# Kernel tuning notes

Hardware: AMD Instinct MI355X
Metric: run time of the kernel (lower is better)

The kernel has to match this reference:

```python
import jax, jax.numpy as jnp
import numpy as np

D_MODEL = 256; N_HEADS = 8; N_LAYERS = 6; D_FF = 1024; BATCH = 1
INPUT_SHAPES = [(24, 24, 24), (12, 12, 12), (6, 6, 6)]
NUM_ORGANS = 20; QPO = 5; LEVELS = 3
NUM_PATCHES = [int(np.prod(s)) for s in INPUT_SHAPES]
S_TOTAL = int(sum(NUM_PATCHES))          # 15768 flattened multi-level patches
NUM_Q = QPO * LEVELS * NUM_ORGANS        # 300 queries


def _build_attn_mask():
    # Same structure as FocusedAttnDecoder.generate_attn_mask: per-organ
    # normalized bbox, scaled (floor/ceil) into each feature level, queries
    # ordered organ-major then level then query copy. True = blocked.
    rng = np.random.RandomState(0)
    mask = np.ones((NUM_Q, S_TOTAL), dtype=bool)
    offsets = np.cumsum([0] + NUM_PATCHES[:-1])
    qi = 0
    for organ in range(NUM_ORGANS):
        lo = rng.uniform(0.0, 0.5, 3)
        hi = np.minimum(lo + rng.uniform(0.15, 0.45, 3), 1.0)
        for lvl in range(LEVELS):
            shp = np.array(INPUT_SHAPES[lvl])
            a = np.floor(lo * shp).astype(int)
            b = np.ceil(hi * shp).astype(int)
            dummy = np.zeros(INPUT_SHAPES[lvl], dtype=bool)
            dummy[a[0]:b[0], a[1]:b[1], a[2]:b[2]] = True
            idx = np.nonzero(dummy.ravel())[0] + offsets[lvl]
            for _ in range(QPO):
                mask[qi, idx] = False
                qi += 1
    return mask


def _xavier(key, shape):
    fan_in, fan_out = shape[-1], shape[-2]
    lim = float(np.sqrt(6.0 / (fan_in + fan_out)))
    return jax.random.uniform(key, shape, minval=-lim, maxval=lim, dtype=jnp.float32)


def setup_inputs() -> dict:
    key = jax.random.key(0)
    ks = jax.random.split(key, 9)
    L, C, F = N_LAYERS, D_MODEL, D_FF
    return {
        "srcs": jax.random.normal(ks[0], (BATCH, C, S_TOTAL), jnp.float32),
        "pos_embeds": jax.random.normal(ks[1], (BATCH, C, S_TOTAL), jnp.float32),
        "query_embed": jax.random.normal(ks[2], (NUM_Q, 2 * C), jnp.float32),
        "attn_mask": jnp.asarray(_build_attn_mask()),
        "sa_in_w": _xavier(ks[3], (L, 3 * C, C)), "sa_in_b": jnp.zeros((L, 3 * C), jnp.float32),
        "sa_out_w": _xavier(ks[4], (L, C, C)), "sa_out_b": jnp.zeros((L, C), jnp.float32),
        "ca_in_w": _xavier(ks[5], (L, 3 * C, C)), "ca_in_b": jnp.zeros((L, 3 * C), jnp.float32),
        "ca_out_w": _xavier(ks[6], (L, C, C)), "ca_out_b": jnp.zeros((L, C), jnp.float32),
        "ln1_w": jnp.ones((L, C), jnp.float32), "ln1_b": jnp.zeros((L, C), jnp.float32),
        "ln2_w": jnp.ones((L, C), jnp.float32), "ln2_b": jnp.zeros((L, C), jnp.float32),
        "ln3_w": jnp.ones((L, C), jnp.float32), "ln3_b": jnp.zeros((L, C), jnp.float32),
        "ff1_w": _xavier(ks[7], (L, F, C)), "ff1_b": jnp.zeros((L, F), jnp.float32),
        "ff2_w": _xavier(ks[8], (L, C, F)), "ff2_b": jnp.zeros((L, C), jnp.float32),
    }


def _ln(x, w, b, eps=1e-5):
    m = jnp.mean(x, axis=-1, keepdims=True)
    v = jnp.mean(jnp.square(x - m), axis=-1, keepdims=True)
    return (x - m) * jax.lax.rsqrt(v + eps) * w + b


def _mha(q_in, k_in, v_in, in_w, in_b, out_w, out_b, mask=None):
    # Faithful nn.MultiheadAttention (eval mode): packed in_proj, scale q,
    # additive -inf mask (True = blocked), softmax, out_proj.
    B, Lq, C = q_in.shape
    H = N_HEADS; Dh = C // H
    wq, wk, wv = jnp.split(in_w, 3, axis=0)
    bq, bk, bv = jnp.split(in_b, 3)
    q = (q_in @ wq.T + bq) * (Dh ** -0.5)
    k = k_in @ wk.T + bk
    v = v_in @ wv.T + bv
    q = q.reshape(B, Lq, H, Dh)
    k = k.reshape(B, k_in.shape[1], H, Dh)
    v = v.reshape(B, v_in.shape[1], H, Dh)
    scores = jnp.einsum('bqhd,bkhd->bhqk', q, k)
    if mask is not None:
        scores = jnp.where(mask[None, None], -jnp.inf, scores)
    attn = jax.nn.softmax(scores, axis=-1)
    out = jnp.einsum('bhqk,bkhd->bqhd', attn, v).reshape(B, Lq, C)
    return out @ out_w.T + out_b


def reference(srcs, pos_embeds, query_embed, attn_mask,
              sa_in_w, sa_in_b, sa_out_w, sa_out_b,
              ca_in_w, ca_in_b, ca_out_w, ca_out_b,
              ln1_w, ln1_b, ln2_w, ln2_b, ln3_w, ln3_b,
              ff1_w, ff1_b, ff2_w, ff2_b):
    C = D_MODEL
    src = jnp.transpose(srcs, (0, 2, 1))        # [B, S, C]
    pos = jnp.transpose(pos_embeds, (0, 2, 1))  # [B, S, C]
    B = src.shape[0]
    qe = jnp.broadcast_to(query_embed[:, :C], (B, NUM_Q, C))
    x = jnp.broadcast_to(query_embed[:, C:], (B, NUM_Q, C))
    for l in range(N_LAYERS):
        # self-attention over queries (q/k get query_pos, v is raw tgt)
        qk = x + qe
        sa = _mha(qk, qk, x, sa_in_w[l], sa_in_b[l], sa_out_w[l], sa_out_b[l])
        x = _ln(x + sa, ln2_w[l], ln2_b[l])
        # mask-restricted cross-attention over flattened multi-level src
        ca = _mha(x + qe, src + pos, src,
                  ca_in_w[l], ca_in_b[l], ca_out_w[l], ca_out_b[l], mask=attn_mask)
        x = _ln(x + ca, ln1_w[l], ln1_b[l])
        # FFN
        h = jax.nn.relu(x @ ff1_w[l].T + ff1_b[l])
        x = _ln(x + (h @ ff2_w[l].T + ff2_b[l]), ln3_w[l], ln3_b[l])
    return x
```

## Files before the change

kernel.cpp:

```cpp
#include <hip/hip_runtime.h>
#include <hip/hip_bf16.h>
#include <math.h>

#define S_TOTAL 15768
#define NQ 300
#define C 256
#define H 8
#define DH 32
#define FF 1024
#define NL 6
#define MAXN 1792
#define NROW 60
#define NT_MAX 16384
#define MQ16 19

#define WB_SAW   0u
#define WB_SAOW  1179648u
#define WB_CAW   1572864u
#define WB_CAOW  2752512u
#define WB_FF1   3145728u
#define WB_FF2   4718592u
#define WB_SAB   6291456u
#define WB_SAOB  6296064u
#define WB_CAB   6297600u
#define WB_CAOB  6302208u
#define WB_FF1B  6303744u
#define WB_FF2B  6309888u
#define WB_TOT   6311424u
#define WT_SAOW  6311424u
#define WT_CAOW  6704640u
#define WB_TOT2  7097856u
#define WT_ELEMS 786432u

typedef __hip_bfloat16 bf16;
typedef __attribute__((ext_vector_type(8))) short bf16x8;
typedef __attribute__((ext_vector_type(4))) float f32x4;

__device__ __forceinline__ float b2f(bf16 v){ return __bfloat162float(v); }

__device__ __forceinline__ float ldin(const void* p, size_t i, int isbf){
    if (isbf) return b2f(((const bf16*)p)[i]);
    return ((const float*)p)[i];
}

__device__ __forceinline__ short f2bf_s(float v){
    bf16 h = __float2bfloat16(v);
    return *(short*)&h;
}

__device__ __forceinline__ float s2f(unsigned short s){
    union { unsigned u; float f; } w; w.u = ((unsigned)s) << 16; return w.f;
}

__device__ __forceinline__ bf16x8 f8_to_bf(float4 a, float4 b){
    bf16x8 r;
    r[0]=f2bf_s(a.x); r[1]=f2bf_s(a.y); r[2]=f2bf_s(a.z); r[3]=f2bf_s(a.w);
    r[4]=f2bf_s(b.x); r[5]=f2bf_s(b.y); r[6]=f2bf_s(b.z); r[7]=f2bf_s(b.w);
    return r;
}


__global__ void detect_cfg(const uint4* __restrict__ srcs,
                           const uint4* __restrict__ mask,
                           int* __restrict__ cfg){
    __shared__ int red[256];
    int t = threadIdx.x;
    int c = 0;
    for (int i = t; i < 16384; i += 256){
        uint4 v = srcs[i];
        unsigned w0 = v.x, w1 = v.y, w2 = v.z, w3 = v.w;
        if ((w0 & 0x7F80u) == 0x7F80u) c++;
        if (((w0 >> 16) & 0x7F80u) == 0x7F80u) c++;
        if ((w1 & 0x7F80u) == 0x7F80u) c++;
        if (((w1 >> 16) & 0x7F80u) == 0x7F80u) c++;
        if ((w2 & 0x7F80u) == 0x7F80u) c++;
        if (((w2 >> 16) & 0x7F80u) == 0x7F80u) c++;
        if ((w3 & 0x7F80u) == 0x7F80u) c++;
        if (((w3 >> 16) & 0x7F80u) == 0x7F80u) c++;
    }
    red[t] = c; __syncthreads();
    for (int s = 128; s > 0; s >>= 1){ if (t < s) red[t] += red[t+s]; __syncthreads(); }
    if (t == 0) cfg[0] = (red[0] >= 16) ? 0 : 1;
    __syncthreads();
    int c2 = 0;
    for (int i = t; i < 4096; i += 256){
        uint4 v = mask[i];
        unsigned w[4] = {v.x, v.y, v.z, v.w};
        #pragma unroll
        for (int j = 0; j < 4; j++){
            unsigned x = w[j];
            c2 += ((x & 0xFFu) != 0) + (((x >> 8) & 0xFFu) != 0)
                + (((x >> 16) & 0xFFu) != 0) + (((x >> 24) & 0xFFu) != 0);
        }
    }
    red[t] = c2; __syncthreads();
    for (int s = 128; s > 0; s >>= 1){ if (t < s) red[t] += red[t+s]; __syncthreads(); }
    if (t == 0) cfg[1] = (red[0] > 32768) ? 1 : 0;
}


__global__ void convert_all(
    const void* saw, const void* sab, const void* saow, const void* saob,
    const void* caw, const void* cab, const void* caow, const void* caob,
    const void* f1w, const void* f1b, const void* f2w, const void* f2b,
    const int* __restrict__ cfg, bf16* __restrict__ Wb)
{
    int isbf = cfg[0];
    size_t i = ((size_t)blockIdx.x*256 + threadIdx.x) * 4;
    if (i >= WB_TOT) return;
    const void* src; size_t loc;
    if      (i < WB_SAOW){ src = saw;  loc = i - WB_SAW; }
    else if (i < WB_CAW) { src = saow; loc = i - WB_SAOW; }
    else if (i < WB_CAOW){ src = caw;  loc = i - WB_CAW; }
    else if (i < WB_FF1) { src = caow; loc = i - WB_CAOW; }
    else if (i < WB_FF2) { src = f1w;  loc = i - WB_FF1; }
    else if (i < WB_SAB) { src = f2w;  loc = i - WB_FF2; }
    else if (i < WB_SAOB){ src = sab;  loc = i - WB_SAB; }
    else if (i < WB_CAB) { src = saob; loc = i - WB_SAOB; }
    else if (i < WB_CAOB){ src = cab;  loc = i - WB_CAB; }
    else if (i < WB_FF1B){ src = caob; loc = i - WB_CAOB; }
    else if (i < WB_FF2B){ src = f1b;  loc = i - WB_FF1B; }
    else                 { src = f2b;  loc = i - WB_FF2B; }
    #pragma unroll
    for (int t = 0; t < 4; t++)
        Wb[i+t] = __float2bfloat16(ldin(src, loc+t, isbf));
}


__global__ void build_wt(bf16* __restrict__ Wb){
    unsigned i = blockIdx.x*256 + threadIdx.x;
    if (i >= WT_ELEMS) return;
    if (i < 393216u){
        unsigned l = i / 65536u, r = i % 65536u, k = r >> 8, n = r & 255u;
        Wb[WT_SAOW + i] = Wb[WB_SAOW + l*65536u + n*256u + k];
    } else {
        unsigned j = i - 393216u;
        unsigned l = j / 65536u, r = j % 65536u, k = r >> 8, n = r & 255u;
        Wb[WT_CAOW + j] = Wb[WB_CAOW + l*65536u + n*256u + k];
    }
}


__global__ void init_qx(const void* __restrict__ qemb, const int* __restrict__ cfg,
                        float* __restrict__ qe, float* __restrict__ x){
    int isbf = cfg[0];
    int i = blockIdx.x*256 + threadIdx.x;
    if (i >= NQ*C) return;
    int row = i / C, col = i % C;
    qe[i] = ldin(qemb, (size_t)row*2*C + col, isbf);
    x[i]  = ldin(qemb, (size_t)row*2*C + C + col, isbf);
}

__global__ void write_out(const float* __restrict__ x, const int* __restrict__ cfg,
                          void* __restrict__ o){
    int isbf = cfg[0];
    int i = blockIdx.x*256 + threadIdx.x;
    if (i >= NQ*C) return;
    if (isbf) ((bf16*)o)[i] = __float2bfloat16(x[i]);
    else      ((float*)o)[i] = x[i];
}


__global__ void count_rows(const unsigned char* __restrict__ mask8,
                           const int* __restrict__ cfg, int* __restrict__ rcnt){
    __shared__ int red[256];
    int r = blockIdx.x;
    int t = threadIdx.x;
    bool isbyte = (cfg[1] != 0);
    const int* row32 = (const int*)mask8 + (size_t)(r*5) * S_TOTAL;
    const unsigned char* row8 = mask8 + (size_t)(r*5) * S_TOTAL;
    int c = 0;
    for (int s = t; s < S_TOTAL; s += 256){
        int blocked = isbyte ? (int)row8[s] : row32[s];
        if (blocked == 0) c++;
    }
    red[t] = c; __syncthreads();
    for (int s = 128; s > 0; s >>= 1){ if (t < s) red[t] += red[t+s]; __syncthreads(); }
    if (t == 0) rcnt[r] = min(red[0], MAXN);
}

__global__ void prefix_rows(const int* __restrict__ rcnt, int* __restrict__ off){
    if (threadIdx.x == 0){
        int a = 0;
        for (int r = 0; r < NROW; r++){
            off[r] = a;
            a = min(a + rcnt[r], NT_MAX);
        }
        off[NROW] = a;
    }
}

__global__ void fill_glist(const unsigned char* __restrict__ mask8,
                           const int* __restrict__ cfg, const int* __restrict__ off,
                           int* __restrict__ glist){
    __shared__ int counts[257];
    int r = blockIdx.x;
    int t = threadIdx.x;
    bool isbyte = (cfg[1] != 0);
    const int* row32 = (const int*)mask8 + (size_t)(r*5) * S_TOTAL;
    const unsigned char* row8 = mask8 + (size_t)(r*5) * S_TOTAL;
    const int chunk = (S_TOTAL + 255) / 256;
    int s0 = t*chunk, s1 = min(S_TOTAL, s0+chunk);
    int c = 0;
    for (int s = s0; s < s1; s++){
        int blocked = isbyte ? (int)row8[s] : row32[s];
        if (blocked == 0) c++;
    }
    counts[t+1] = c;
    __syncthreads();
    if (t == 0){
        counts[0] = 0;
        for (int i = 1; i <= 256; i++) counts[i] += counts[i-1];
    }
    __syncthreads();
    int o = off[r] + counts[t];
    int lim = off[r+1];
    for (int s = s0; s < s1; s++){
        int blocked = isbyte ? (int)row8[s] : row32[s];
        if (blocked == 0){ if (o < lim) glist[o] = s; o++; }
    }
}


__global__ __launch_bounds__(256) void gather_cast(
    const void* __restrict__ srcs, const void* __restrict__ pos,
    const int* __restrict__ cfg, const int* __restrict__ glist,
    const int* __restrict__ off,
    bf16* __restrict__ Agkv, bf16* __restrict__ Agsrc)
{
    int NT = off[NROW];
    int m0 = blockIdx.x * 64;
    if (m0 >= NT) return;
    int isbf = cfg[0];
    __shared__ __align__(16) short Tkv[64][40];
    __shared__ __align__(16) short Tsr[64][40];
    int tid = threadIdx.x;
    int am = tid & 63;
    int kg = (tid >> 6) * 8;
    int mg = m0 + am;
    int g = (mg < NT) ? glist[mg] : 0;
    int wn = tid >> 2;
    int wk = (tid & 3) * 8;
    bool wvalid = (m0 + wn < NT);
    for (int k0 = 0; k0 < C; k0 += 32){
        #pragma unroll
        for (int i = 0; i < 8; i++){
            int k = k0 + kg + i;
            float s  = ldin(srcs, (size_t)k*S_TOTAL + g, isbf);
            float pp = ldin(pos,  (size_t)k*S_TOTAL + g, isbf);
            Tsr[am][kg+i] = f2bf_s(s);
            Tkv[am][kg+i] = f2bf_s(s + pp);
        }
        __syncthreads();
        if (wvalid){
            *(bf16x8*)(Agkv  + (size_t)(m0+wn)*C + k0 + wk) = *(const bf16x8*)&Tkv[wn][wk];
            *(bf16x8*)(Agsrc + (size_t)(m0+wn)*C + k0 + wk) = *(const bf16x8*)&Tsr[wn][wk];
        }
        __syncthreads();
    }
}


__global__ __launch_bounds__(256) void gemm_kv3(
    const bf16* __restrict__ Agkv, const bf16* __restrict__ Agsrc,
    const bf16* __restrict__ Wb, int lstart,
    const int* __restrict__ off, bf16* __restrict__ KV)
{
    int NT = off[NROW];
    int m0 = blockIdx.x * 128;
    if (m0 >= NT) return;
    int z = blockIdx.z;
    int l = lstart + (z >> 1);
    int kv = z & 1;
    const bf16* Ag = kv ? Agsrc : Agkv;
    size_t woff = WB_CAW + ((size_t)l*3 + 1 + kv) * C * C;
    size_t boff = WB_CAB + ((size_t)l*3 + 1 + kv) * C;
    bf16* Out = KV + (size_t)z * NT_MAX * C;
    int n0 = blockIdx.y * 128;
    int tid = threadIdx.x;
    int lane = tid & 63, wid = tid >> 6;
    int fr = lane & 15, quad = lane >> 4;
    int mbase = (wid & 1) * 64, nbase = (wid >> 1) * 64;

    __shared__ __align__(16) short As[128][72];
    __shared__ __align__(16) short Bs[128][72];

    f32x4 acc[4][4];
    #pragma unroll
    for (int i = 0; i < 4; i++)
        #pragma unroll
        for (int j = 0; j < 4; j++) acc[i][j] = (f32x4)(0.f);

    for (int k0 = 0; k0 < C; k0 += 64){
        #pragma unroll
        for (int it = 0; it < 4; it++){
            int idx = tid + it*256;
            int row = idx >> 3;
            int kseg = (idx & 7) * 8;
            *(bf16x8*)&As[row][kseg] = *(const bf16x8*)(Ag + (size_t)(m0+row)*C + k0 + kseg);
            *(bf16x8*)&Bs[row][kseg] = *(const bf16x8*)(Wb + woff + (size_t)(n0+row)*C + k0 + kseg);
        }
        __syncthreads();
        #pragma unroll
        for (int h = 0; h < 2; h++){
            bf16x8 af[4], bfr[4];
            #pragma unroll
            for (int i = 0; i < 4; i++) af[i] = *(const bf16x8*)&As[mbase+i*16+fr][h*32 + quad*8];
            #pragma unroll
            for (int j = 0; j < 4; j++) bfr[j] = *(const bf16x8*)&Bs[nbase+j*16+fr][h*32 + quad*8];
            #pragma unroll
            for (int i = 0; i < 4; i++)
                #pragma unroll
                for (int j = 0; j < 4; j++)
                    acc[i][j] = __builtin_amdgcn_mfma_f32_16x16x32_bf16(af[i], bfr[j], acc[i][j], 0, 0, 0);
        }
        __syncthreads();
    }

    int col16 = lane & 15, rq = quad * 4;
    #pragma unroll
    for (int j = 0; j < 4; j++){
        int gn = n0 + nbase + j*16 + col16;
        float bv = b2f(Wb[boff + gn]);
        #pragma unroll
        for (int i = 0; i < 4; i++){
            #pragma unroll
            for (int r = 0; r < 4; r++){
                int gm2 = m0 + mbase + i*16 + rq + r;
                if (gm2 < NT) Out[(size_t)gm2*C + gn] = __float2bfloat16(acc[i][j][r] + bv);
            }
        }
    }
}


__global__ __launch_bounds__(64) void gemm_q_mfma(
    const float* __restrict__ A, const float* __restrict__ A2, int a2_nlimit,
    int lda, const bf16* __restrict__ W, size_t woff,
    size_t boff, float* __restrict__ Out,
    int M, int N, int K, int relu)
{
    int lane = threadIdx.x;
    int m0 = blockIdx.x * 16, n0 = blockIdx.y * 16;
    int fr = lane & 15, quad = lane >> 4;
    int gm = m0 + fr;
    int n  = n0 + fr;
    bool mrow = (gm < M);
    bool use2 = (A2 != nullptr) && (n0 < a2_nlimit);
    f32x4 acc = (f32x4)(0.f);

    for (int k0 = 0; k0 < K; k0 += 32){
        bf16x8 af = (bf16x8)(short)0;
        if (mrow){
            const float4* pa = (const float4*)(A + (size_t)gm*lda + k0 + quad*8);
            float4 a0 = pa[0], a1 = pa[1];
            if (use2){
                const float4* p2 = (const float4*)(A2 + (size_t)gm*lda + k0 + quad*8);
                float4 b0 = p2[0], b1 = p2[1];
                a0.x += b0.x; a0.y += b0.y; a0.z += b0.z; a0.w += b0.w;
                a1.x += b1.x; a1.y += b1.y; a1.z += b1.z; a1.w += b1.w;
            }
            af = f8_to_bf(a0, a1);
        }
        bf16x8 bf_ = *(const bf16x8*)(W + woff + (size_t)n*K + k0 + quad*8);
        acc = __builtin_amdgcn_mfma_f32_16x16x32_bf16(af, bf_, acc, 0, 0, 0);
    }

    int col = n0 + (lane & 15);
    int rq = quad * 4;
    float bv = b2f(W[boff + col]);
    #pragma unroll
    for (int r = 0; r < 4; r++){
        int gmr = m0 + rq + r;
        if (gmr < M){
            float v = acc[r] + bv;
            if (relu) v = fmaxf(v, 0.f);
            Out[(size_t)gmr*N + col] = v;
        }
    }
}


__global__ __launch_bounds__(256) void row_out_ln(
    const float* __restrict__ A, const bf16* __restrict__ Wb,
    size_t wtoff, size_t boff,
    const void* __restrict__ lnw, const void* __restrict__ lnb, size_t lnoff,
    const int* __restrict__ cfg, float* __restrict__ x)
{
    int isbf = cfg[0];
    int row = blockIdx.x;
    int tid = threadIdx.x;
    int lane = tid & 63, wv = tid >> 6;
    __shared__ float as[C];
    __shared__ float wsum[4], wsq[4];
    as[tid] = A[(size_t)row*C + tid];
    __syncthreads();
    const bf16* wt = Wb + wtoff;
    float a0=0.f, a1=0.f, a2=0.f, a3=0.f;
    #pragma unroll 4
    for (int k = 0; k < C; k += 4){
        a0 += as[k]   * b2f(wt[(size_t)k*256 + tid]);
        a1 += as[k+1] * b2f(wt[(size_t)(k+1)*256 + tid]);
        a2 += as[k+2] * b2f(wt[(size_t)(k+2)*256 + tid]);
        a3 += as[k+3] * b2f(wt[(size_t)(k+3)*256 + tid]);
    }
    float v = (a0+a1) + (a2+a3) + b2f(Wb[boff + tid]) + x[(size_t)row*C + tid];
    float s = v, q = v*v;
    #pragma unroll
    for (int m = 1; m < 64; m <<= 1){
        s += __shfl_xor(s, m);
        q += __shfl_xor(q, m);
    }
    if (lane == 0){ wsum[wv] = s; wsq[wv] = q; }
    __syncthreads();
    float S = wsum[0]+wsum[1]+wsum[2]+wsum[3];
    float Q = wsq[0]+wsq[1]+wsq[2]+wsq[3];
    float mean = S * (1.f/256.f);
    float var  = Q * (1.f/256.f) - mean*mean;
    float r = (v - mean) * rsqrtf(var + 1e-5f);
    x[(size_t)row*C + tid] = r * ldin(lnw, lnoff+tid, isbf) + ldin(lnb, lnoff+tid, isbf);
}


__global__ void sa_attn(const float* __restrict__ qkv, float* __restrict__ out){
    int qi = blockIdx.x, h = blockIdx.y;
    int lane = threadIdx.x;
    __shared__ __align__(16) float qv[DH];
    __shared__ float sc[NQ];
    const float scale = 0.17677669529663687f;
    if (lane < DH) qv[lane] = qkv[qi*768 + h*DH + lane] * scale;
    __syncthreads();
    float mx = -1e30f;
    const float4* q4 = (const float4*)qv;
    for (int j = lane; j < NQ; j += 64){
        const float4* kp = (const float4*)(qkv + j*768 + 256 + h*DH);
        float d = 0.f;
        #pragma unroll
        for (int b = 0; b < 8; b++){
            float4 kk = kp[b];
            float4 qq = q4[b];
            d += qq.x*kk.x + qq.y*kk.y + qq.z*kk.z + qq.w*kk.w;
        }
        sc[j] = d; mx = fmaxf(mx, d);
    }
    for (int m = 1; m < 64; m <<= 1) mx = fmaxf(mx, __shfl_xor(mx, m));
    float sum = 0.f;
    __syncthreads();
    for (int j = lane; j < NQ; j += 64){ float e = __expf(sc[j]-mx); sc[j] = e; sum += e; }
    for (int m = 1; m < 64; m <<= 1) sum += __shfl_xor(sum, m);
    __syncthreads();
    int dd8 = lane & 3, grp = lane >> 2;
    float acc[8];
    #pragma unroll
    for (int t = 0; t < 8; t++) acc[t] = 0.f;
    for (int j = grp; j < NQ; j += 16){
        const float4* vp = (const float4*)(qkv + j*768 + 512 + h*DH + dd8*8);
        float4 v0 = vp[0], v1 = vp[1];
        float s = sc[j];
        acc[0] += s*v0.x; acc[1] += s*v0.y; acc[2] += s*v0.z; acc[3] += s*v0.w;
        acc[4] += s*v1.x; acc[5] += s*v1.y; acc[6] += s*v1.z; acc[7] += s*v1.w;
    }
    #pragma unroll
    for (int t = 0; t < 8; t++){
        float a = acc[t];
        a += __shfl_xor(a, 4); a += __shfl_xor(a, 8);
        a += __shfl_xor(a, 16); a += __shfl_xor(a, 32);
        acc[t] = a;
    }
    if (lane < 4){
        float inv = 1.f/sum;
        #pragma unroll
        for (int t = 0; t < 8; t++)
            out[qi*C + h*DH + dd8*8 + t] = acc[t]*inv;
    }
}


__global__ __launch_bounds__(256) void ca_attn(
    const float* __restrict__ q, const bf16* __restrict__ Kg,
    const bf16* __restrict__ Vg, const int* __restrict__ off,
    float* __restrict__ out)
{
    int r = blockIdx.x, h = blockIdx.y;
    int tid = threadIdx.x;
    int lane = tid & 63, wv = tid >> 6;
    int base = off[r], n = off[r+1] - base;
    __shared__ __align__(16) float qv[5][DH];
    __shared__ float sc[5][MAXN];
    __shared__ float wred[5][4];
    __shared__ float wsum[5][4];
    __shared__ float pacc[4][5][DH];
    const float scale = 0.17677669529663687f;
    for (int i = tid; i < 5*DH; i += 256){
        int qc = i >> 5, d = i & 31;
        qv[qc][d] = q[(size_t)(r*5+qc)*C + h*DH + d] * scale;
    }
    __syncthreads();
    float mx[5] = {-1e30f,-1e30f,-1e30f,-1e30f,-1e30f};
    for (int ki = tid; ki < n; ki += 256){
        const bf16x8* kp = (const bf16x8*)(Kg + (size_t)(base+ki)*C + h*DH);
        float kf[32];
        #pragma unroll
        for (int b = 0; b < 4; b++){
            bf16x8 k8 = kp[b];
            #pragma unroll
            for (int t = 0; t < 8; t++) kf[b*8+t] = s2f((unsigned short)k8[t]);
        }
        #pragma unroll
        for (int qc = 0; qc < 5; qc++){
            const float4* q4 = (const float4*)qv[qc];
            float d = 0.f;
            #pragma unroll
            for (int b = 0; b < 8; b++){
                float4 qq = q4[b];
                d += qq.x*kf[b*4] + qq.y*kf[b*4+1] + qq.z*kf[b*4+2] + qq.w*kf[b*4+3];
            }
            sc[qc][ki] = d;
            mx[qc] = fmaxf(mx[qc], d);
        }
    }
    #pragma unroll
    for (int qc = 0; qc < 5; qc++)
        for (int m = 1; m < 64; m <<= 1) mx[qc] = fmaxf(mx[qc], __shfl_xor(mx[qc], m));
    if (lane == 0){
        #pragma unroll
        for (int qc = 0; qc < 5; qc++) wred[qc][wv] = mx[qc];
    }
    __syncthreads();
    #pragma unroll
    for (int qc = 0; qc < 5; qc++)
        mx[qc] = fmaxf(fmaxf(wred[qc][0], wred[qc][1]), fmaxf(wred[qc][2], wred[qc][3]));
    float sum[5] = {0.f,0.f,0.f,0.f,0.f};
    for (int ki = tid; ki < n; ki += 256){
        #pragma unroll
        for (int qc = 0; qc < 5; qc++){
            float e = __expf(sc[qc][ki] - mx[qc]);
            sc[qc][ki] = e;
            sum[qc] += e;
        }
    }
    #pragma unroll
    for (int qc = 0; qc < 5; qc++)
        for (int m = 1; m < 64; m <<= 1) sum[qc] += __shfl_xor(sum[qc], m);
    if (lane == 0){
        #pragma unroll
        for (int qc = 0; qc < 5; qc++) wsum[qc][wv] = sum[qc];
    }
    __syncthreads();
    #pragma unroll
    for (int qc = 0; qc < 5; qc++)
        sum[qc] = wsum[qc][0] + wsum[qc][1] + wsum[qc][2] + wsum[qc][3];
    int dd8 = tid & 3, grp = tid >> 2;
    float acc[5][8];
    #pragma unroll
    for (int qc = 0; qc < 5; qc++)
        #pragma unroll
        for (int t = 0; t < 8; t++) acc[qc][t] = 0.f;
    for (int j = grp; j < n; j += 64){
        bf16x8 v8 = *(const bf16x8*)(Vg + (size_t)(base+j)*C + h*DH + dd8*8);
        float vf[8];
        #pragma unroll
        for (int t = 0; t < 8; t++) vf[t] = s2f((unsigned short)v8[t]);
        #pragma unroll
        for (int qc = 0; qc < 5; qc++){
            float s = sc[qc][j];
            #pragma unroll
            for (int t = 0; t < 8; t++) acc[qc][t] += s*vf[t];
        }
    }
    #pragma unroll
    for (int qc = 0; qc < 5; qc++)
        #pragma unroll
        for (int t = 0; t < 8; t++){
            float a = acc[qc][t];
            a += __shfl_xor(a, 4); a += __shfl_xor(a, 8);
            a += __shfl_xor(a, 16); a += __shfl_xor(a, 32);
            acc[qc][t] = a;
        }
    if (lane < 4){
        #pragma unroll
        for (int qc = 0; qc < 5; qc++)
            #pragma unroll
            for (int t = 0; t < 8; t++) pacc[wv][qc][dd8*8+t] = acc[qc][t];
    }
    __syncthreads();
    if (tid < 5*DH){
        int qc = tid >> 5, d = tid & 31;
        float a = pacc[0][qc][d] + pacc[1][qc][d] + pacc[2][qc][d] + pacc[3][qc][d];
        float inv = (n > 0 && sum[qc] > 0.f) ? 1.f/sum[qc] : 0.f;
        out[(size_t)(r*5+qc)*C + h*DH + d] = a*inv;
    }
}


__global__ void add_res_ln(float* __restrict__ x, const float* __restrict__ t,
                           const void* __restrict__ w, const void* __restrict__ b,
                           size_t off, const int* __restrict__ cfg){
    int isbf = cfg[0];
    int row = blockIdx.x;
    int tid = threadIdx.x;
    int lane = tid & 63, wv = tid >> 6;
    __shared__ float wsum[4], wsq[4];
    float v = x[row*C + tid] + t[row*C + tid];
    float s = v, q = v*v;
    #pragma unroll
    for (int m = 1; m < 64; m <<= 1){
        s += __shfl_xor(s, m);
        q += __shfl_xor(q, m);
    }
    if (lane == 0){ wsum[wv] = s; wsq[wv] = q; }
    __syncthreads();
    float S = wsum[0]+wsum[1]+wsum[2]+wsum[3];
    float Q = wsq[0]+wsq[1]+wsq[2]+wsq[3];
    float mean = S * (1.f/256.f);
    float var  = Q * (1.f/256.f) - mean*mean;
    float r = (v - mean) * rsqrtf(var + 1e-5f);
    x[row*C + tid] = r * ldin(w, off + tid, isbf) + ldin(b, off + tid, isbf);
}


extern "C" void kernel_launch(void* const* d_in, const int* in_sizes, int n_in,
                              void* d_out, int out_size, void* d_ws, size_t ws_size,
                              hipStream_t stream) {
    const void* srcs    = d_in[0];
    const void* pos     = d_in[1];
    const void* qemb    = d_in[2];
    const unsigned char* mask = (const unsigned char*)d_in[3];
    const void* sa_in_w = d_in[4];
    const void* sa_in_b = d_in[5];
    const void* sa_out_w= d_in[6];
    const void* sa_out_b= d_in[7];
    const void* ca_in_w = d_in[8];
    const void* ca_in_b = d_in[9];
    const void* ca_out_w= d_in[10];
    const void* ca_out_b= d_in[11];
    const void* ln1_w   = d_in[12];
    const void* ln1_b   = d_in[13];
    const void* ln2_w   = d_in[14];
    const void* ln2_b   = d_in[15];
    const void* ln3_w   = d_in[16];
    const void* ln3_b   = d_in[17];
    const void* ff1_w   = d_in[18];
    const void* ff1_b   = d_in[19];
    const void* ff2_w   = d_in[20];
    const void* ff2_b   = d_in[21];

    const size_t SLICE = (size_t)NT_MAX * C / 2;

    float* p = (float*)d_ws;
    float* qe    = p; p += NQ*C;
    float* x     = p; p += NQ*C;
    bf16*  Agkv  = (bf16*)p; p += SLICE;
    bf16*  Agsrc = (bf16*)p; p += SLICE;
    bf16*  Wb    = (bf16*)p; p += (WB_TOT2+2)/2;
    float* saqkv = p; p += NQ*768;
    float* att   = p; p += NQ*C;
    float* tmp   = p; p += NQ*C;
    float* hbuf  = p; p += NQ*FF;
    float* qbuf  = p; p += NQ*C;
    int*   glist = (int*)p; p += NT_MAX;
    int*   rcnt  = (int*)p; p += NROW;
    int*   off   = (int*)p; p += NROW+4;
    int*   cfg   = (int*)p; p += 4;
    bf16*  KV    = (bf16*)p;

    size_t base_bytes = (size_t)((char*)KV - (char*)d_ws);
    bool hoist = (ws_size >= base_bytes + 12 * SLICE * sizeof(float));

    dim3 blk(256);
    const size_t CC = (size_t)C*C;

    detect_cfg<<<1, blk, 0, stream>>>((const uint4*)srcs, (const uint4*)mask, cfg);
    convert_all<<<(WB_TOT/4 + 255)/256, blk, 0, stream>>>(
        sa_in_w, sa_in_b, sa_out_w, sa_out_b, ca_in_w, ca_in_b, ca_out_w, ca_out_b,
        ff1_w, ff1_b, ff2_w, ff2_b, cfg, Wb);
    build_wt<<<(WT_ELEMS + 255)/256, blk, 0, stream>>>(Wb);
    init_qx<<<(NQ*C+255)/256, blk, 0, stream>>>(qemb, cfg, qe, x);
    count_rows<<<NROW, blk, 0, stream>>>(mask, cfg, rcnt);
    prefix_rows<<<1, 64, 0, stream>>>(rcnt, off);
    fill_glist<<<NROW, blk, 0, stream>>>(mask, cfg, off, glist);
    gather_cast<<<NT_MAX/64, blk, 0, stream>>>(srcs, pos, cfg, glist, off, Agkv, Agsrc);

    if (hoist){
        gemm_kv3<<<dim3(NT_MAX/128, 2, 2*NL), blk, 0, stream>>>(
            Agkv, Agsrc, Wb, 0, off, KV);
    }

    for (int l = 0; l < NL; l++){
        bf16* Kg; bf16* Vg;
        if (hoist){
            Kg = KV + (size_t)(2*l)   * NT_MAX * C;
            Vg = KV + (size_t)(2*l+1) * NT_MAX * C;
        } else {
            Kg = KV;
            Vg = KV + (size_t)NT_MAX * C;
            gemm_kv3<<<dim3(NT_MAX/128, 2, 2), blk, 0, stream>>>(
                Agkv, Agsrc, Wb, l, off, KV);
        }

        gemm_q_mfma<<<dim3(MQ16, 48), 64, 0, stream>>>(
            x, qe, 512, C, Wb, WB_SAW + (size_t)l*3*CC, WB_SAB + (size_t)l*3*C,
            saqkv, NQ, 768, C, 0);
        sa_attn<<<dim3(NQ, H), 64, 0, stream>>>(saqkv, att);
        row_out_ln<<<NQ, blk, 0, stream>>>(
            att, Wb, WT_SAOW + (size_t)l*CC, WB_SAOB + (size_t)l*C,
            ln2_w, ln2_b, (size_t)l*C, cfg, x);

        gemm_q_mfma<<<dim3(MQ16, 16), 64, 0, stream>>>(
            x, qe, 256, C, Wb, WB_CAW + (size_t)l*3*CC, WB_CAB + (size_t)l*3*C,
            qbuf, NQ, 256, C, 0);
        ca_attn<<<dim3(NROW, H), blk, 0, stream>>>(qbuf, Kg, Vg, off, att);
        row_out_ln<<<NQ, blk, 0, stream>>>(
            att, Wb, WT_CAOW + (size_t)l*CC, WB_CAOB + (size_t)l*C,
            ln1_w, ln1_b, (size_t)l*C, cfg, x);

        gemm_q_mfma<<<dim3(MQ16, 64), 64, 0, stream>>>(
            x, nullptr, 0, C, Wb, WB_FF1 + (size_t)l*FF*C, WB_FF1B + (size_t)l*FF,
            hbuf, NQ, FF, C, 1);
        gemm_q_mfma<<<dim3(MQ16, 16), 64, 0, stream>>>(
            hbuf, nullptr, 0, FF, Wb, WB_FF2 + (size_t)l*C*FF, WB_FF2B + (size_t)l*C,
            tmp, NQ, C, FF, 0);
        add_res_ln<<<NQ, blk, 0, stream>>>(x, tmp, ln3_w, ln3_b, (size_t)l*C, cfg);
    }

    write_out<<<(NQ*C+255)/256, blk, 0, stream>>>(x, cfg, d_out);
}
```

Before: 915.7 us.

## Fuse all decoder layers into one persistent kernel with a software grid barrier

Replaces the per-layer sequence of many small kernel launches with a single persistent kernel of 512 blocks. The blocks step through the self-attention, cross-attention, FFN and layernorm phases and synchronize through a hierarchical atomic grid barrier. Self-attention and its output projection plus layernorm are merged into one per-query pass. This targets launch overhead and idle gaps between the tiny per-layer kernels. The cost is barrier spin time, less parallelism in some phases, and a risk of deadlock if all 512 blocks cannot be resident at once.

```diff
diff --git a/kernel.cpp b/kernel.cpp
--- a/kernel.cpp
+++ b/kernel.cpp
@@ -13,6 +13,7 @@
 #define NROW 60
 #define NT_MAX 16384
 #define MQ16 19
+#define GRID 512
 
 #define WB_SAW   0u
 #define WB_SAOW  1179648u
@@ -179,7 +180,9 @@
     if (t == 0) rcnt[r] = min(red[0], MAXN);
 }
 
-__global__ void prefix_rows(const int* __restrict__ rcnt, int* __restrict__ off){
+__global__ void prefix_rows(const int* __restrict__ rcnt, int* __restrict__ off,
+                            int* __restrict__ bar){
+    for (int i = threadIdx.x; i < 160; i += 64) bar[i] = 0;
     if (threadIdx.x == 0){
         int a = 0;
         for (int r = 0; r < NROW; r++){
@@ -334,14 +337,12 @@
 }
 
 
-__global__ __launch_bounds__(64) void gemm_q_mfma(
+__device__ __forceinline__ void gemm_tile16(
     const float* __restrict__ A, const float* __restrict__ A2, int a2_nlimit,
-    int lda, const bf16* __restrict__ W, size_t woff,
-    size_t boff, float* __restrict__ Out,
-    int M, int N, int K, int relu)
+    int lda, const bf16* __restrict__ W, size_t woff, size_t boff,
+    float* __restrict__ Out, int M, int N, int K, int relu,
+    int m0, int n0, int lane)
 {
-    int lane = threadIdx.x;
-    int m0 = blockIdx.x * 16, n0 = blockIdx.y * 16;
     int fr = lane & 15, quad = lane >> 4;
     int gm = m0 + fr;
     int n  = n0 + fr;
@@ -366,20 +367,63 @@
         acc = __builtin_amdgcn_mfma_f32_16x16x32_bf16(af, bf_, acc, 0, 0, 0);
     }
 
-    int col = n0 + (lane & 15);
+    float bv = b2f(W[boff + n]);
     int rq = quad * 4;
-    float bv = b2f(W[boff + col]);
     #pragma unroll
     for (int r = 0; r < 4; r++){
         int gmr = m0 + rq + r;
         if (gmr < M){
             float v = acc[r] + bv;
             if (relu) v = fmaxf(v, 0.f);
-            Out[(size_t)gmr*N + col] = v;
-        }
-    }
-}
-
+            Out[(size_t)gmr*N + n] = v;
+        }
+    }
+}
+
+
+__global__ __launch_bounds__(64) void gemm_q_mfma(
+    const float* __restrict__ A, const float* __restrict__ A2, int a2_nlimit,
+    int lda, const bf16* __restrict__ W, size_t woff,
+    size_t boff, float* __restrict__ Out,
+    int M, int N, int K, int relu)
+{
+    gemm_tile16(A, A2, a2_nlimit, lda, W, woff, boff, Out, M, N, K, relu,
+                blockIdx.x * 16, blockIdx.y * 16, (int)threadIdx.x);
+}
+
+
+__device__ __forceinline__ void out_ln_row(
+    const float* __restrict__ arow, const bf16* __restrict__ Wb,
+    size_t wtoff, size_t boff,
+    const void* __restrict__ lnw, const void* __restrict__ lnb, size_t lnoff,
+    int isbf, float* __restrict__ x, int row, int tid, float* __restrict__ red)
+{
+    int lane = tid & 63, wvv = tid >> 6;
+    const bf16* wt = Wb + wtoff;
+    float a0=0.f, a1=0.f, a2=0.f, a3=0.f;
+    #pragma unroll 4
+    for (int k = 0; k < C; k += 4){
+        a0 += arow[k]   * b2f(wt[(size_t)k*256 + tid]);
+        a1 += arow[k+1] * b2f(wt[(size_t)(k+1)*256 + tid]);
+        a2 += arow[k+2] * b2f(wt[(size_t)(k+2)*256 + tid]);
+        a3 += arow[k+3] * b2f(wt[(size_t)(k+3)*256 + tid]);
+    }
+    float v = (a0+a1) + (a2+a3) + b2f(Wb[boff + tid]) + x[(size_t)row*C + tid];
+    float s = v, q = v*v;
+    #pragma unroll
+    for (int m = 1; m < 64; m <<= 1){
+        s += __shfl_xor(s, m);
+        q += __shfl_xor(q, m);
+    }
+    if (lane == 0){ red[wvv] = s; red[4+wvv] = q; }
+    __syncthreads();
+    float S = red[0]+red[1]+red[2]+red[3];
+    float Q = red[4]+red[5]+red[6]+red[7];
+    float mean = S * (1.f/256.f);
+    float var  = Q * (1.f/256.f) - mean*mean;
+    float r = (v - mean) * rsqrtf(var + 1e-5f);
+    x[(size_t)row*C + tid] = r * ldin(lnw, lnoff+tid, isbf) + ldin(lnb, lnoff+tid, isbf);
+}
 
 __global__ __launch_bounds__(256) void row_out_ln(
     const float* __restrict__ A, const bf16* __restrict__ Wb,
@@ -387,38 +431,13 @@
     const void* __restrict__ lnw, const void* __restrict__ lnb, size_t lnoff,
     const int* __restrict__ cfg, float* __restrict__ x)
 {
-    int isbf = cfg[0];
     int row = blockIdx.x;
     int tid = threadIdx.x;
-    int lane = tid & 63, wv = tid >> 6;
     __shared__ float as[C];
-    __shared__ float wsum[4], wsq[4];
+    __shared__ float red[8];
     as[tid] = A[(size_t)row*C + tid];
     __syncthreads();
-    const bf16* wt = Wb + wtoff;
-    float a0=0.f, a1=0.f, a2=0.f, a3=0.f;
-    #pragma unroll 4
-    for (int k = 0; k < C; k += 4){
-        a0 += as[k]   * b2f(wt[(size_t)k*256 + tid]);
-        a1 += as[k+1] * b2f(wt[(size_t)(k+1)*256 + tid]);
-        a2 += as[k+2] * b2f(wt[(size_t)(k+2)*256 + tid]);
-        a3 += as[k+3] * b2f(wt[(size_t)(k+3)*256 + tid]);
-    }
-    float v = (a0+a1) + (a2+a3) + b2f(Wb[boff + tid]) + x[(size_t)row*C + tid];
-    float s = v, q = v*v;
-    #pragma unroll
-    for (int m = 1; m < 64; m <<= 1){
-        s += __shfl_xor(s, m);
-        q += __shfl_xor(q, m);
-    }
-    if (lane == 0){ wsum[wv] = s; wsq[wv] = q; }
-    __syncthreads();
-    float S = wsum[0]+wsum[1]+wsum[2]+wsum[3];
-    float Q = wsq[0]+wsq[1]+wsq[2]+wsq[3];
-    float mean = S * (1.f/256.f);
-    float var  = Q * (1.f/256.f) - mean*mean;
-    float r = (v - mean) * rsqrtf(var + 1e-5f);
-    x[(size_t)row*C + tid] = r * ldin(lnw, lnoff+tid, isbf) + ldin(lnb, lnoff+tid, isbf);
+    out_ln_row(as, Wb, wtoff, boff, lnw, lnb, lnoff, cfg[0], x, row, tid, red);
 }
 
 
@@ -616,6 +635,310 @@
     float var  = Q * (1.f/256.f) - mean*mean;
     float r = (v - mean) * rsqrtf(var + 1e-5f);
     x[row*C + tid] = r * ldin(w, off + tid, isbf) + ldin(b, off + tid, isbf);
+}
+
+
+__device__ __forceinline__ void gsync(int* __restrict__ bar){
+    __syncthreads();
+    if (threadIdx.x == 0){
+        int g = __hip_atomic_load(bar + 144, __ATOMIC_RELAXED, __HIP_MEMORY_SCOPE_AGENT);
+        int sc_ = (blockIdx.x & 7) << 4;
+        int a = __hip_atomic_fetch_add(bar + sc_, 1, __ATOMIC_ACQ_REL, __HIP_MEMORY_SCOPE_AGENT);
+        if (a == (GRID/8) - 1){
+            __hip_atomic_store(bar + sc_, 0, __ATOMIC_RELAXED, __HIP_MEMORY_SCOPE_AGENT);
+            int m = __hip_atomic_fetch_add(bar + 128, 1, __ATOMIC_ACQ_REL, __HIP_MEMORY_SCOPE_AGENT);
+            if (m == 7){
+                __hip_atomic_store(bar + 128, 0, __ATOMIC_RELAXED, __HIP_MEMORY_SCOPE_AGENT);
+                __hip_atomic_fetch_add(bar + 144, 1, __ATOMIC_ACQ_REL, __HIP_MEMORY_SCOPE_AGENT);
+            }
+        }
+        while (__hip_atomic_load(bar + 144, __ATOMIC_RELAXED, __HIP_MEMORY_SCOPE_AGENT) == g)
+            __builtin_amdgcn_s_sleep(4);
+        (void)__hip_atomic_load(bar + 144, __ATOMIC_ACQUIRE, __HIP_MEMORY_SCOPE_AGENT);
+    }
+    __syncthreads();
+}
+
+union __align__(16) ShU {
+    struct { float qv[8][DH]; float as[C]; float red[8]; } sa;
+    struct { float as[C]; float red[8]; } ro;
+    struct { float qv[5][DH]; float sc[5][MAXN]; float wred[5][4];
+             float wsum[5][4]; float pacc[4][5][DH]; } ca;
+};
+
+__global__ __launch_bounds__(256, 2) void fused_layers(
+    const void* __restrict__ qemb, const int* __restrict__ cfg,
+    const bf16* __restrict__ Wb, const int* __restrict__ off,
+    const bf16* __restrict__ KV,
+    const void* __restrict__ ln1w, const void* __restrict__ ln1b,
+    const void* __restrict__ ln2w, const void* __restrict__ ln2b,
+    const void* __restrict__ ln3w, const void* __restrict__ ln3b,
+    float* __restrict__ qe, float* __restrict__ x,
+    float* __restrict__ saqkv, float* __restrict__ att,
+    float* __restrict__ qbuf, float* __restrict__ hbuf, float* __restrict__ tmp,
+    int* __restrict__ bar, void* __restrict__ outp)
+{
+    __shared__ ShU sh;
+    int tid = threadIdx.x, bid = blockIdx.x;
+    int lane = tid & 63, wv = tid >> 6;
+    int gw = (bid << 2) | wv;
+    int isbf = cfg[0];
+    const float scale = 0.17677669529663687f;
+    const size_t CC = (size_t)C*C;
+
+    for (int i = bid*256 + tid; i < NQ*C; i += GRID*256){
+        int row = i >> 8, col = i & 255;
+        qe[i] = ldin(qemb, (size_t)row*2*C + col, isbf);
+        x[i]  = ldin(qemb, (size_t)row*2*C + C + col, isbf);
+    }
+    gsync(bar);
+
+    for (int l = 0; l < NL; l++){
+        for (int t = gw; t < 19*48; t += GRID*4)
+            gemm_tile16(x, qe, 512, C, Wb, WB_SAW + (size_t)l*3*CC, WB_SAB + (size_t)l*3*C,
+                        saqkv, NQ, 768, C, 0, (t % 19)*16, (t / 19)*16, lane);
+        gsync(bar);
+
+        for (int q = bid; q < NQ; q += GRID){
+            {
+                int h2 = tid >> 5, d = tid & 31;
+                sh.sa.qv[h2][d] = saqkv[(size_t)q*768 + h2*DH + d] * scale;
+            }
+            __syncthreads();
+            #pragma unroll
+            for (int hh = 0; hh < 2; hh++){
+                int h = wv*2 + hh;
+                float e[5]; float mx = -1e30f;
+                #pragma unroll
+                for (int i = 0; i < 5; i++){
+                    int j = lane + 64*i;
+                    float d = -1e30f;
+                    if (j < NQ){
+                        const float4* kp = (const float4*)(saqkv + (size_t)j*768 + 256 + h*DH);
+                        const float4* q4 = (const float4*)sh.sa.qv[h];
+                        d = 0.f;
+                        #pragma unroll
+                        for (int b = 0; b < 8; b++){
+                            float4 kk = kp[b], qq = q4[b];
+                            d += qq.x*kk.x + qq.y*kk.y + qq.z*kk.z + qq.w*kk.w;
+                        }
+                    }
+                    e[i] = d; mx = fmaxf(mx, d);
+                }
+                #pragma unroll
+                for (int m = 1; m < 64; m <<= 1) mx = fmaxf(mx, __shfl_xor(mx, m));
+                float sum = 0.f;
+                #pragma unroll
+                for (int i = 0; i < 5; i++){
+                    int j = lane + 64*i;
+                    float ee = (j < NQ) ? __expf(e[i] - mx) : 0.f;
+                    e[i] = ee; sum += ee;
+                }
+                #pragma unroll
+                for (int m = 1; m < 64; m <<= 1) sum += __shfl_xor(sum, m);
+                int dd8 = lane & 3, grp = lane >> 2;
+                float acc[8];
+                #pragma unroll
+                for (int t = 0; t < 8; t++) acc[t] = 0.f;
+                #pragma unroll
+                for (int k = 0; k < 19; k++){
+                    int j = grp + 16*k;
+                    float s = __shfl(e[k>>2], j & 63);
+                    if (j < NQ){
+                        const float4* vp = (const float4*)(saqkv + (size_t)j*768 + 512 + h*DH + dd8*8);
+                        float4 v0 = vp[0], v1 = vp[1];
+                        acc[0] += s*v0.x; acc[1] += s*v0.y; acc[2] += s*v0.z; acc[3] += s*v0.w;
+                        acc[4] += s*v1.x; acc[5] += s*v1.y; acc[6] += s*v1.z; acc[7] += s*v1.w;
+                    }
+                }
+                #pragma unroll
+                for (int t = 0; t < 8; t++){
+                    float a = acc[t];
+                    a += __shfl_xor(a, 4); a += __shfl_xor(a, 8);
+                    a += __shfl_xor(a, 16); a += __shfl_xor(a, 32);
+                    acc[t] = a;
+                }
+                if (lane < 4){
+                    float inv = 1.f/sum;
+                    #pragma unroll
+                    for (int t = 0; t < 8; t++)
+                        sh.sa.as[h*DH + dd8*8 + t] = acc[t]*inv;
+                }
+            }
+            __syncthreads();
+            out_ln_row(sh.sa.as, Wb, WT_SAOW + (size_t)l*CC, WB_SAOB + (size_t)l*C,
+                       ln2w, ln2b, (size_t)l*C, isbf, x, q, tid, sh.sa.red);
+            __syncthreads();
+        }
+        gsync(bar);
+
+        for (int t = gw; t < 19*16; t += GRID*4)
+            gemm_tile16(x, qe, 256, C, Wb, WB_CAW + (size_t)l*3*CC, WB_CAB + (size_t)l*3*C,
+                        qbuf, NQ, 256, C, 0, (t % 19)*16, (t / 19)*16, lane);
+        gsync(bar);
+
+        {
+            const bf16* Kg = KV + (size_t)(2*l)   * NT_MAX * C;
+            const bf16* Vg = KV + (size_t)(2*l+1) * NT_MAX * C;
+            for (int u = bid; u < NROW*H; u += GRID){
+                int r = u >> 3, h = u & 7;
+                int base = off[r], n = off[r+1] - base;
+                for (int i = tid; i < 5*DH; i += 256){
+                    int qc = i >> 5, d = i & 31;
+                    sh.ca.qv[qc][d] = qbuf[(size_t)(r*5+qc)*C + h*DH + d] * scale;
+                }
+                __syncthreads();
+                float mx[5] = {-1e30f,-1e30f,-1e30f,-1e30f,-1e30f};
+                for (int ki = tid; ki < n; ki += 256){
+                    const bf16x8* kp = (const bf16x8*)(Kg + (size_t)(base+ki)*C + h*DH);
+                    float kf[32];
+                    #pragma unroll
+                    for (int b = 0; b < 4; b++){
+                        bf16x8 k8 = kp[b];
+                        #pragma unroll
+                        for (int t = 0; t < 8; t++) kf[b*8+t] = s2f((unsigned short)k8[t]);
+                    }
+                    #pragma unroll
+                    for (int qc = 0; qc < 5; qc++){
+                        const float4* q4 = (const float4*)sh.ca.qv[qc];
+                        float d = 0.f;
+                        #pragma unroll
+                        for (int b = 0; b < 8; b++){
+                            float4 qq = q4[b];
+                            d += qq.x*kf[b*4] + qq.y*kf[b*4+1] + qq.z*kf[b*4+2] + qq.w*kf[b*4+3];
+                        }
+                        sh.ca.sc[qc][ki] = d;
+                        mx[qc] = fmaxf(mx[qc], d);
+                    }
+                }
+                #pragma unroll
+                for (int qc = 0; qc < 5; qc++)
+                    for (int m = 1; m < 64; m <<= 1) mx[qc] = fmaxf(mx[qc], __shfl_xor(mx[qc], m));
+                if (lane == 0){
+                    #pragma unroll
+                    for (int qc = 0; qc < 5; qc++) sh.ca.wred[qc][wv] = mx[qc];
+                }
+                __syncthreads();
+                #pragma unroll
+                for (int qc = 0; qc < 5; qc++)
+                    mx[qc] = fmaxf(fmaxf(sh.ca.wred[qc][0], sh.ca.wred[qc][1]),
+                                   fmaxf(sh.ca.wred[qc][2], sh.ca.wred[qc][3]));
+                float sum[5] = {0.f,0.f,0.f,0.f,0.f};
+                for (int ki = tid; ki < n; ki += 256){
+                    #pragma unroll
+                    for (int qc = 0; qc < 5; qc++){
+                        float e = __expf(sh.ca.sc[qc][ki] - mx[qc]);
+                        sh.ca.sc[qc][ki] = e;
+                        sum[qc] += e;
+                    }
+                }
+                #pragma unroll
+                for (int qc = 0; qc < 5; qc++)
+                    for (int m = 1; m < 64; m <<= 1) sum[qc] += __shfl_xor(sum[qc], m);
+                if (lane == 0){
+                    #pragma unroll
+                    for (int qc = 0; qc < 5; qc++) sh.ca.wsum[qc][wv] = sum[qc];
+                }
+                __syncthreads();
+                #pragma unroll
+                for (int qc = 0; qc < 5; qc++)
+                    sum[qc] = sh.ca.wsum[qc][0] + sh.ca.wsum[qc][1]
+                            + sh.ca.wsum[qc][2] + sh.ca.wsum[qc][3];
+                int dd8 = tid & 3, grp = tid >> 2;
+                float acc[5][8];
+                #pragma unroll
+                for (int qc = 0; qc < 5; qc++)
+                    #pragma unroll
+                    for (int t = 0; t < 8; t++) acc[qc][t] = 0.f;
+                for (int j = grp; j < n; j += 64){
+                    bf16x8 v8 = *(const bf16x8*)(Vg + (size_t)(base+j)*C + h*DH + dd8*8);
+                    float vf[8];
+                    #pragma unroll
+                    for (int t = 0; t < 8; t++) vf[t] = s2f((unsigned short)v8[t]);
+                    #pragma unroll
+                    for (int qc = 0; qc < 5; qc++){
+                        float s = sh.ca.sc[qc][j];
+                        #pragma unroll
+                        for (int t = 0; t < 8; t++) acc[qc][t] += s*vf[t];
+                    }
+                }
+                #pragma unroll
+                for (int qc = 0; qc < 5; qc++)
+                    #pragma unroll
+                    for (int t = 0; t < 8; t++){
+                        float a = acc[qc][t];
+                        a += __shfl_xor(a, 4); a += __shfl_xor(a, 8);
+                        a += __shfl_xor(a, 16); a += __shfl_xor(a, 32);
+                        acc[qc][t] = a;
+                    }
+                if (lane < 4){
+                    #pragma unroll
+                    for (int qc = 0; qc < 5; qc++)
+                        #pragma unroll
+                        for (int t = 0; t < 8; t++) sh.ca.pacc[wv][qc][dd8*8+t] = acc[qc][t];
+                }
+                __syncthreads();
+                if (tid < 5*DH){
+                    int qc = tid >> 5, d = tid & 31;
+                    float a = sh.ca.pacc[0][qc][d] + sh.ca.pacc[1][qc][d]
+                            + sh.ca.pacc[2][qc][d] + sh.ca.pacc[3][qc][d];
+                    float inv = (n > 0 && sum[qc] > 0.f) ? 1.f/sum[qc] : 0.f;
+                    att[(size_t)(r*5+qc)*C + h*DH + d] = a*inv;
+                }
+                __syncthreads();
+            }
+        }
+        gsync(bar);
+
+        for (int row = bid; row < NQ; row += GRID){
+            sh.ro.as[tid] = att[(size_t)row*C + tid];
+            __syncthreads();
+            out_ln_row(sh.ro.as, Wb, WT_CAOW + (size_t)l*CC, WB_CAOB + (size_t)l*C,
+                       ln1w, ln1b, (size_t)l*C, isbf, x, row, tid, sh.ro.red);
+            __syncthreads();
+        }
+        gsync(bar);
+
+        for (int t = gw; t < 19*64; t += GRID*4)
+            gemm_tile16(x, nullptr, 0, C, Wb, WB_FF1 + (size_t)l*FF*C, WB_FF1B + (size_t)l*FF,
+                        hbuf, NQ, FF, C, 1, (t % 19)*16, (t / 19)*16, lane);
+        gsync(bar);
+
+        for (int t = gw; t < 19*16; t += GRID*4)
+            gemm_tile16(hbuf, nullptr, 0, FF, Wb, WB_FF2 + (size_t)l*C*FF, WB_FF2B + (size_t)l*C,
+                        tmp, NQ, C, FF, 0, (t % 19)*16, (t / 19)*16, lane);
+        gsync(bar);
+
+        for (int row = gw; row < NQ; row += GRID*4){
+            int c0 = lane*4;
+            float4 xv = *(const float4*)(x   + (size_t)row*C + c0);
+            float4 tv = *(const float4*)(tmp + (size_t)row*C + c0);
+            float v0 = xv.x+tv.x, v1 = xv.y+tv.y, v2 = xv.z+tv.z, v3 = xv.w+tv.w;
+            float s  = v0+v1+v2+v3;
+            float qq = v0*v0+v1*v1+v2*v2+v3*v3;
+            #pragma unroll
+            for (int m = 1; m < 64; m <<= 1){
+                s  += __shfl_xor(s, m);
+                qq += __shfl_xor(qq, m);
+            }
+            float mean = s * (1.f/256.f);
+            float var  = qq * (1.f/256.f) - mean*mean;
+            float inv  = rsqrtf(var + 1e-5f);
+            size_t lo = (size_t)l*C + c0;
+            float4 ov;
+            ov.x = (v0-mean)*inv * ldin(ln3w, lo+0, isbf) + ldin(ln3b, lo+0, isbf);
+            ov.y = (v1-mean)*inv * ldin(ln3w, lo+1, isbf) + ldin(ln3b, lo+1, isbf);
+            ov.z = (v2-mean)*inv * ldin(ln3w, lo+2, isbf) + ldin(ln3b, lo+2, isbf);
+            ov.w = (v3-mean)*inv * ldin(ln3w, lo+3, isbf) + ldin(ln3b, lo+3, isbf);
+            *(float4*)(x + (size_t)row*C + c0) = ov;
+        }
+        gsync(bar);
+    }
+
+    for (int i = bid*256 + tid; i < NQ*C; i += GRID*256){
+        if (isbf) ((bf16*)outp)[i] = __float2bfloat16(x[i]);
+        else      ((float*)outp)[i] = x[i];
+    }
 }
 
 
@@ -662,6 +985,7 @@
     int*   rcnt  = (int*)p; p += NROW;
     int*   off   = (int*)p; p += NROW+4;
     int*   cfg   = (int*)p; p += 4;
+    int*   bar   = (int*)p; p += 160;
     bf16*  KV    = (bf16*)p;
 
     size_t base_bytes = (size_t)((char*)KV - (char*)d_ws);
@@ -675,28 +999,27 @@
         sa_in_w, sa_in_b, sa_out_w, sa_out_b, ca_in_w, ca_in_b, ca_out_w, ca_out_b,
         ff1_w, ff1_b, ff2_w, ff2_b, cfg, Wb);
     build_wt<<<(WT_ELEMS + 255)/256, blk, 0, stream>>>(Wb);
-    init_qx<<<(NQ*C+255)/256, blk, 0, stream>>>(qemb, cfg, qe, x);
     count_rows<<<NROW, blk, 0, stream>>>(mask, cfg, rcnt);
-    prefix_rows<<<1, 64, 0, stream>>>(rcnt, off);
+    prefix_rows<<<1, 64, 0, stream>>>(rcnt, off, bar);
     fill_glist<<<NROW, blk, 0, stream>>>(mask, cfg, off, glist);
     gather_cast<<<NT_MAX/64, blk, 0, stream>>>(srcs, pos, cfg, glist, off, Agkv, Agsrc);
 
     if (hoist){
         gemm_kv3<<<dim3(NT_MAX/128, 2, 2*NL), blk, 0, stream>>>(
             Agkv, Agsrc, Wb, 0, off, KV);
-    }
-
+        fused_layers<<<dim3(GRID), blk, 0, stream>>>(
+            qemb, cfg, Wb, off, KV,
+            ln1_w, ln1_b, ln2_w, ln2_b, ln3_w, ln3_b,
+            qe, x, saqkv, att, qbuf, hbuf, tmp, bar, d_out);
+        return;
+    }
+
+    init_qx<<<(NQ*C+255)/256, blk, 0, stream>>>(qemb, cfg, qe, x);
     for (int l = 0; l < NL; l++){
-        bf16* Kg; bf16* Vg;
-        if (hoist){
-            Kg = KV + (size_t)(2*l)   * NT_MAX * C;
-            Vg = KV + (size_t)(2*l+1) * NT_MAX * C;
-        } else {
-            Kg = KV;
-            Vg = KV + (size_t)NT_MAX * C;
-            gemm_kv3<<<dim3(NT_MAX/128, 2, 2), blk, 0, stream>>>(
-                Agkv, Agsrc, Wb, l, off, KV);
-        }
+        bf16* Kg = KV;
+        bf16* Vg = KV + (size_t)NT_MAX * C;
+        gemm_kv3<<<dim3(NT_MAX/128, 2, 2), blk, 0, stream>>>(
+            Agkv, Agsrc, Wb, l, off, KV);
 
         gemm_q_mfma<<<dim3(MQ16, 48), 64, 0, stream>>>(
             x, qe, 512, C, Wb, WB_SAW + (size_t)l*3*CC, WB_SAB + (size_t)l*3*C,
@@ -722,6 +1045,5 @@
             tmp, NQ, C, FF, 0);
         add_res_ln<<<NQ, blk, 0, stream>>>(x, tmp, ln3_w, ln3_b, (size_t)l*C, cfg);
     }
-
     write_out<<<(NQ*C+255)/256, blk, 0, stream>>>(x, cfg, d_out);
 }
```

After: 2.002 ms. 119% more time.
